# Optimization experiments

Hardware: AMD Instinct MI355X
Metric: run time of the kernel (lower is better)

The kernel has to match this reference:

```python
import jax, jax.numpy as jnp
import numpy as np

B, K, H = 512, 160, 256
ALPHA = 0.5          # fgw_alpha
TEMP = 2.0           # consistency temperature
MAX_SPAN = 30        # max_span_len
L_FGW, L_SPAN, L_CONS = 0.1, 0.5, 0.3


def setup_inputs() -> dict:
    key = jax.random.key(0)
    ks = jax.random.split(key, 12)
    gamma = jax.random.uniform(ks[0], (B, K, K), jnp.float32) / K  # transport-plan scale
    return {
        "en_node_emb": jax.random.normal(ks[1], (B, K, H), jnp.float32),
        "vi_node_emb": jax.random.normal(ks[2], (B, K, H), jnp.float32),
        "gamma": gamma,
        "D_en": jax.random.uniform(ks[3], (B, K, K), jnp.float32),
        "D_vi": jax.random.uniform(ks[4], (B, K, K), jnp.float32),
        "M": jax.random.uniform(ks[5], (B, K, K), jnp.float32),
        "en_start": jax.random.randint(ks[6], (B,), 0, K, jnp.int64 if jax.config.read('jax_enable_x64') else jnp.int32),
        "en_end": jax.random.randint(ks[7], (B,), 0, K, jnp.int64 if jax.config.read('jax_enable_x64') else jnp.int32),
        "w_start": jax.random.normal(ks[8], (H, 1), jnp.float32) * 0.02,
        "b_start": jnp.zeros((1,), jnp.float32),
        "w_end": jax.random.normal(ks[9], (H, 1), jnp.float32) * 0.02,
        "b_end": jnp.zeros((1,), jnp.float32),
    }


def _qa_head(emb, w_s, b_s, w_e, b_e):
    # emb: (B,K,H) -> logits (B,K)
    start = (emb @ w_s).squeeze(-1) + b_s
    end = (emb @ w_e).squeeze(-1) + b_e
    return start, end


def _ce(logits, labels):
    # mean cross-entropy, labels always valid after clamping
    logp = jax.nn.log_softmax(logits, axis=-1)
    return -jnp.take_along_axis(logp, labels[:, None], axis=-1).squeeze(-1)


def _fgw_loss(gamma, D_en, D_vi, M, alpha):
    w = jnp.sum(M * gamma, axis=(1, 2))
    p = gamma.sum(axis=2)  # (B,K)
    q = gamma.sum(axis=1)  # (B,K)
    gw1 = jnp.einsum('bij,bi,bj->b', D_en ** 2, p, p)
    gw2 = jnp.einsum('bij,bi,bj->b', D_vi ** 2, q, q)
    t = jnp.einsum('bik,bkl->bil', D_en, gamma)       # C1 @ g
    t = jnp.einsum('bil,bjl->bij', t, D_vi)           # (C1 @ g) @ C2^T
    gw3 = jnp.sum(t * gamma, axis=(1, 2))
    return jnp.mean(alpha * (gw1 + gw2 - 2.0 * gw3) + (1.0 - alpha) * w)


def _decode_span(gamma, en_start, en_end, k, max_span):
    # pseudo-label decode (no-grad in original) -> (B,) int start/end
    idx = jnp.arange(k)
    s = jnp.clip(en_start, 0, k - 1)
    e = jnp.maximum(s, jnp.clip(en_end, 0, k - 1))
    row_mask = (idx[None, :] >= s[:, None]) & (idx[None, :] <= e[:, None])  # (B,K)
    vi_score = jnp.einsum('bi,bij->bj', row_mask.astype(gamma.dtype), gamma)  # (B,K)
    pair = vi_score[:, :, None] + vi_score[:, None, :]  # (B, si, ei)
    span = idx[None, :] - idx[:, None]                  # ei - si
    valid = (span >= 0) & (span <= max_span)
    pair = jnp.where(valid[None], pair, -jnp.inf)
    flat = jnp.argmax(pair.reshape(pair.shape[0], -1), axis=-1)
    best_s, best_e = flat // k, flat % k
    unanswerable = (en_start == 0) & (en_end == 0)
    best_s = jnp.where(unanswerable, 0, best_s)
    best_e = jnp.where(unanswerable, 0, best_e)
    return best_s, best_e


def _kl_batchmean(vi_logp, en_logp):
    # KL(target=exp(en_logp) || vi) with torch kl_div(batchmean) semantics
    p = jnp.exp(en_logp)
    return jnp.sum(p * (en_logp - vi_logp)) / p.shape[0]


def reference(en_node_emb, vi_node_emb, gamma, D_en, D_vi, M, en_start, en_end,
              w_start, b_start, w_end, b_end):
    en_sl, en_el = _qa_head(en_node_emb, w_start, b_start, w_end, b_end)
    vi_sl, vi_el = _qa_head(vi_node_emb, w_start, b_start, w_end, b_end)

    # QA loss (EN supervised, positions clamped into [0, K-1])
    s_lab = jnp.clip(en_start, 0, K - 1)
    e_lab = jnp.clip(en_end, 0, K - 1)
    l_qa = (jnp.mean(_ce(en_sl, s_lab)) + jnp.mean(_ce(en_el, e_lab))) / 2.0

    # FGW alignment
    l_fgw = _fgw_loss(gamma, D_en, D_vi, M, ALPHA)

    # Span projection (pseudo labels via stop-gradient on gamma)
    ps, pe = _decode_span(jax.lax.stop_gradient(gamma), en_start, en_end, K, MAX_SPAN)
    answerable = ((en_start > 0) | (en_end > 0)).astype(jnp.float32)
    n_ans = jnp.sum(answerable)
    ce_span = (_ce(vi_sl, ps) + _ce(vi_el, pe)) / 2.0  # (B,)
    l_span = jnp.where(n_ans > 0, jnp.sum(ce_span * answerable) / jnp.maximum(n_ans, 1.0), 0.0)

    # Consistency (EN detached)
    en_s_log = jax.nn.log_softmax(jax.lax.stop_gradient(en_sl) / TEMP, axis=-1)
    en_e_log = jax.nn.log_softmax(jax.lax.stop_gradient(en_el) / TEMP, axis=-1)
    vi_s_log = jax.nn.log_softmax(vi_sl / TEMP, axis=-1)
    vi_e_log = jax.nn.log_softmax(vi_el / TEMP, axis=-1)
    l_cons = TEMP ** 2 * (_kl_batchmean(vi_s_log, en_s_log) + _kl_batchmean(vi_e_log, en_e_log)) / 2.0

    total = l_qa + L_FGW * l_fgw + L_SPAN * l_span + L_CONS * l_cons
    return total, l_qa, l_fgw, l_span, l_cons
```

## Files before the change

### kernel.cpp

```cpp
#include <hip/hip_runtime.h>

#define Bn 512
#define Kn 160
#define Hn 256
#define ALPHA 0.5f
#define MAX_SPAN 30
#define L_FGW 0.1f
#define L_SPAN 0.5f
#define L_CONS 0.3f
#define KP 16
#define NP 10

typedef __bf16 bf16x8 __attribute__((ext_vector_type(8)));
typedef float f32x16 __attribute__((ext_vector_type(16)));
typedef float f32x4v __attribute__((ext_vector_type(4)));

struct PhS {
  float prow[160][41];
  float qcol[16][160];
  float vcol[16][160];
  float psh[160], qsh[160], vscsh[160];
  float esh[160], eeh[160], vssh[160], veh[160];
  float wsh[16], g1sh[16], g2sh[16];
  float bv[256];
  int bidx[256];
  int pspe[2];
};
struct FgS {
  __bf16 sDen[2][2][Kn][8];
  __bf16 sG[2][2][Kn][8];
  __bf16 sGT[2][2][Kn][8];
  __bf16 sVT[2][2][Kn][8];
  float red[16];
};

__device__ __forceinline__ void wg_barrier() {
  asm volatile("s_waitcnt lgkmcnt(0)" ::: "memory");
  __builtin_amdgcn_s_barrier();
  __builtin_amdgcn_sched_barrier(0);
}

__global__ __launch_bounds__(1024, 4) void mega_k(
    const float* __restrict__ en, const float* __restrict__ vi,
    const float* __restrict__ w_s, const float* __restrict__ b_s,
    const float* __restrict__ w_e, const float* __restrict__ b_e,
    const float* __restrict__ gam, const float* __restrict__ M,
    const float* __restrict__ Den, const float* __restrict__ Dvi,
    const int* __restrict__ enst, const int* __restrict__ enen,
    float* __restrict__ sp1) {
  __shared__ __align__(16) char shraw[sizeof(PhS)];
  PhS& S = *(PhS*)shraw;
  FgS& F = *(FgS*)shraw;
  int b = blockIdx.x;
  int tid = threadIdx.x;
  int wv = tid >> 6, lane = tid & 63;
  const float* gam_b = gam + (size_t)b * 25600;
  const float* m_b   = M   + (size_t)b * 25600;
  const float* den_b = Den + (size_t)b * 25600;
  const float* dvi_b = Dvi + (size_t)b * 25600;
  int s0 = enst[b], e0 = enen[b];
  int s = min(max(s0, 0), Kn - 1);
  int e = max(s, min(max(e0, 0), Kn - 1));
  bool actA = tid < 640;
  int rm = tid / 40, c = tid - 40 * rm;

  float4 ws4 = *(const float4*)(w_s + lane * 4);
  float4 we4 = *(const float4*)(w_e + lane * 4);
  float bs0 = b_s[0], be0 = b_e[0];
  const float* en_b = en + (size_t)b * 40960;
  const float* vi_b = vi + (size_t)b * 40960;
  float q4[4] = {0.f,0.f,0.f,0.f}, v4[4] = {0.f,0.f,0.f,0.f};
  float wloc = 0.f;
  #pragma unroll
  for (int it = 0; it < 10; ++it) {
    int crow = wv * 10 + it;
    f32x4v ev = __builtin_nontemporal_load((const f32x4v*)(en_b + (size_t)crow * 256 + lane * 4));
    f32x4v vv = __builtin_nontemporal_load((const f32x4v*)(vi_b + (size_t)crow * 256 + lane * 4));
    if (actA) {
      int r = 16 * it + rm;
      float4 g = *(const float4*)(gam_b + (size_t)r * 160 + 4 * c);
      f32x4v m = __builtin_nontemporal_load((const f32x4v*)(m_b + (size_t)r * 160 + 4 * c));
      wloc += m[0]*g.x + m[1]*g.y + m[2]*g.z + m[3]*g.w;
      S.prow[r][c] = g.x + g.y + g.z + g.w;
      q4[0]+=g.x; q4[1]+=g.y; q4[2]+=g.z; q4[3]+=g.w;
      float f = (r >= s && r <= e) ? 1.f : 0.f;
      v4[0]+=f*g.x; v4[1]+=f*g.y; v4[2]+=f*g.z; v4[3]+=f*g.w;
    }
    float a0 = ev[0]*ws4.x + ev[1]*ws4.y + ev[2]*ws4.z + ev[3]*ws4.w;
    float a1 = ev[0]*we4.x + ev[1]*we4.y + ev[2]*we4.z + ev[3]*we4.w;
    float a2 = vv[0]*ws4.x + vv[1]*ws4.y + vv[2]*ws4.z + vv[3]*ws4.w;
    float a3 = vv[0]*we4.x + vv[1]*we4.y + vv[2]*we4.z + vv[3]*we4.w;
    #pragma unroll
    for (int o = 32; o; o >>= 1) {
      a0 += __shfl_xor(a0, o); a1 += __shfl_xor(a1, o);
      a2 += __shfl_xor(a2, o); a3 += __shfl_xor(a3, o);
    }
    if (lane == 0) {
      S.esh[crow] = a0 + bs0;  S.eeh[crow] = a1 + be0;
      S.vssh[crow] = a2 + bs0; S.veh[crow] = a3 + be0;
    }
  }
  if (actA) {
    #pragma unroll
    for (int j = 0; j < 4; ++j) { S.qcol[rm][4*c+j] = q4[j]; S.vcol[rm][4*c+j] = v4[j]; }
  }
  #pragma unroll
  for (int o = 32; o; o >>= 1) wloc += __shfl_xor(wloc, o);
  if (lane == 0) S.wsh[wv] = wloc;
  __syncthreads();
  if (tid < 160) {
    float sp = 0.f;
    #pragma unroll 8
    for (int c2 = 0; c2 < 40; ++c2) sp += S.prow[tid][c2];
    S.psh[tid] = sp;
    float sq = 0.f, sv = 0.f;
    #pragma unroll 4
    for (int k = 0; k < 16; ++k) { sq += S.qcol[k][tid]; sv += S.vcol[k][tid]; }
    S.qsh[tid] = sq;
    S.vscsh[tid] = sv;
  }
  __syncthreads();

  float g1loc = 0.f, g2loc = 0.f;
  if (actA) {
    float pc0=S.psh[4*c], pc1=S.psh[4*c+1], pc2=S.psh[4*c+2], pc3=S.psh[4*c+3];
    float qc0=S.qsh[4*c], qc1=S.qsh[4*c+1], qc2=S.qsh[4*c+2], qc3=S.qsh[4*c+3];
    #pragma unroll
    for (int k = 0; k < 10; ++k) {
      int r = 16 * k + rm;
      float4 d = *(const float4*)(den_b + (size_t)r * 160 + 4 * c);
      g1loc += S.psh[r] * (d.x*d.x*pc0 + d.y*d.y*pc1 + d.z*d.z*pc2 + d.w*d.w*pc3);
      float4 v = *(const float4*)(dvi_b + (size_t)r * 160 + 4 * c);
      g2loc += S.qsh[r] * (v.x*v.x*qc0 + v.y*v.y*qc1 + v.z*v.z*qc2 + v.w*v.w*qc3);
    }
  }
  #pragma unroll
  for (int o = 32; o; o >>= 1) { g1loc += __shfl_xor(g1loc, o); g2loc += __shfl_xor(g2loc, o); }
  if (lane == 0) { S.g1sh[wv] = g1loc; S.g2sh[wv] = g2loc; }
  __syncthreads();

  float best = -1e30f;
  int bfl = 0x7fffffff;
  if (tid < 160) {
    float vsi = S.vscsh[tid];
    int hi = min(tid + MAX_SPAN, Kn - 1);
    for (int ei = tid; ei <= hi; ++ei) {
      float v = vsi + S.vscsh[ei];
      if (v > best) { best = v; bfl = tid * Kn + ei; }
    }
  }
  if (tid < 256) { S.bv[tid] = best; S.bidx[tid] = bfl; }
  for (int st = 128; st > 0; st >>= 1) {
    __syncthreads();
    if (tid < st) {
      float v2 = S.bv[tid + st]; int i2 = S.bidx[tid + st];
      if (v2 > S.bv[tid] || (v2 == S.bv[tid] && i2 < S.bidx[tid])) { S.bv[tid] = v2; S.bidx[tid] = i2; }
    }
  }
  if (tid == 0) {
    int fl = S.bidx[0];
    int ps = fl / Kn, pe = fl - (fl / Kn) * Kn;
    if (s0 == 0 && e0 == 0) { ps = 0; pe = 0; }
    S.pspe[0] = ps; S.pspe[1] = pe;
    float sw = 0.f, s1 = 0.f, s2 = 0.f;
    #pragma unroll
    for (int i = 0; i < 16; ++i) { sw += S.wsh[i]; s1 += S.g1sh[i]; s2 += S.g2sh[i]; }
    float* o = sp1 + (size_t)b * 12;
    o[4] = sw; o[7] = s1; o[8] = s2;
  }
  __syncthreads();
  if (wv == 0) {
    float xes[3], xee[3], xvs[3], xve[3];
    #pragma unroll
    for (int j = 0; j < 3; ++j) {
      int idx = lane + 64 * j;
      bool val = idx < Kn;
      xes[j] = val ? S.esh[idx] : -1e30f;
      xee[j] = val ? S.eeh[idx] : -1e30f;
      xvs[j] = val ? S.vssh[idx] : -1e30f;
      xve[j] = val ? S.veh[idx] : -1e30f;
    }
    auto wlse = [&](float x0, float x1, float x2) -> float {
      float m = fmaxf(fmaxf(x0, x1), x2);
      #pragma unroll
      for (int o = 32; o; o >>= 1) m = fmaxf(m, __shfl_xor(m, o));
      float su = expf(x0 - m) + expf(x1 - m) + expf(x2 - m);
      #pragma unroll
      for (int o = 32; o; o >>= 1) su += __shfl_xor(su, o);
      return m + logf(su);
    };
    float l_es = wlse(xes[0], xes[1], xes[2]);
    float l_ee = wlse(xee[0], xee[1], xee[2]);
    float l_vs = wlse(xvs[0], xvs[1], xvs[2]);
    float l_ve = wlse(xve[0], xve[1], xve[2]);
    float lT_es = wlse(xes[0]*0.5f, xes[1]*0.5f, xes[2]*0.5f);
    float lT_ee = wlse(xee[0]*0.5f, xee[1]*0.5f, xee[2]*0.5f);
    float lT_vs = wlse(xvs[0]*0.5f, xvs[1]*0.5f, xvs[2]*0.5f);
    float lT_ve = wlse(xve[0]*0.5f, xve[1]*0.5f, xve[2]*0.5f);
    float kls = 0.f, kle = 0.f;
    #pragma unroll
    for (int j = 0; j < 3; ++j) {
      int idx = lane + 64 * j;
      if (idx < Kn) {
        float aa = xes[j]*0.5f - lT_es;
        float bb = xvs[j]*0.5f - lT_vs;
        kls += expf(aa) * (aa - bb);
        float cc = xee[j]*0.5f - lT_ee;
        float dd = xve[j]*0.5f - lT_ve;
        kle += expf(cc) * (cc - dd);
      }
    }
    #pragma unroll
    for (int o = 32; o; o >>= 1) { kls += __shfl_xor(kls, o); kle += __shfl_xor(kle, o); }
    if (lane == 0) {
      int sl = min(max(s0, 0), Kn - 1);
      int el = min(max(e0, 0), Kn - 1);
      float* o = sp1 + (size_t)b * 12;
      o[0] = l_es - S.esh[sl];
      o[1] = l_ee - S.eeh[el];
      o[2] = kls;
      o[3] = kle;
      bool answerable = (s0 > 0) || (e0 > 0);
      float ce = 0.5f * ((l_vs - S.vssh[S.pspe[0]]) + (l_ve - S.veh[S.pspe[1]]));
      o[5] = answerable ? ce : 0.f;
      o[6] = answerable ? 1.f : 0.f;
    }
  }
  __syncthreads();

  bool rm0 = tid < 640;
  const float* s0p;
  __bf16 *d00, *d01;
  if (rm0) {
    int op = tid >= 320 ? 1 : 0;
    int fr = tid - 320 * op;
    int cc = fr >= 160 ? 1 : 0;
    int r = fr - 160 * cc;
    s0p = (op ? gam_b : den_b) + (size_t)r * 160 + 8 * cc;
    d00 = op ? &F.sG[0][cc][r][0] : &F.sDen[0][cc][r][0];
    d01 = op ? &F.sG[1][cc][r][0] : &F.sDen[1][cc][r][0];
  } else {
    int f3 = tid - 640;
    int op = f3 >= 320 ? 1 : 0;
    int f4 = f3 - 320 * op;
    int cc = f4 >= 160 ? 1 : 0;
    int j = f4 - 160 * cc;
    s0p = (op ? dvi_b : gam_b) + (size_t)(8 * cc) * 160 + j;
    d00 = op ? &F.sVT[0][cc][j][0] : &F.sGT[0][cc][j][0];
    d01 = op ? &F.sVT[1][cc][j][0] : &F.sGT[1][cc][j][0];
  }
  bool act1 = tid < 256;
  int f5 = tid + 64;
  int cc1 = f5 >= 160 ? 1 : 0;
  int j1 = f5 - 160 * cc1;
  const float* s1p = dvi_b + (size_t)(8 * cc1) * 160 + j1;
  __bf16* d10 = &F.sVT[0][cc1][j1][0];
  __bf16* d11 = &F.sVT[1][cc1][j1][0];

  float vA0[8], vA1[8], vB0[8], vB1[8];
  auto load0 = [&](int p, float* v) {
    if (rm0) {
      const float* sp = s0p + p * KP;
      float4 x = *(const float4*)sp;
      float4 y = *(const float4*)(sp + 4);
      v[0]=x.x; v[1]=x.y; v[2]=x.z; v[3]=x.w;
      v[4]=y.x; v[5]=y.y; v[6]=y.z; v[7]=y.w;
    } else {
      const float* sp = s0p + (size_t)p * KP * 160;
      #pragma unroll
      for (int e2 = 0; e2 < 8; ++e2) v[e2] = sp[(size_t)e2 * 160];
    }
  };
  auto load1 = [&](int p, float* v) {
    if (!act1) return;
    const float* sp = s1p + (size_t)p * KP * 160;
    #pragma unroll
    for (int e2 = 0; e2 < 8; ++e2) v[e2] = sp[(size_t)e2 * 160];
  };
  auto wr = [&](const float* v0, const float* v1, __bf16* w0, __bf16* w1) {
    bf16x8 wv2;
    #pragma unroll
    for (int e2 = 0; e2 < 8; ++e2) wv2[e2] = (__bf16)v0[e2];
    *(bf16x8*)w0 = wv2;
    if (act1) {
      bf16x8 wv3;
      #pragma unroll
      for (int e2 = 0; e2 < 8; ++e2) wv3[e2] = (__bf16)v1[e2];
      *(bf16x8*)w1 = wv3;
    }
  };

  int ra = lane & 31, cc2 = lane >> 5;
  int t0 = wv;
  int ti0 = t0 / 5, tj0 = t0 - 5 * (t0 / 5);
  int rowa0 = ti0 * 32 + ra, rowb0 = tj0 * 32 + ra;
  int t1 = wv + 16;
  bool val1t = t1 < 25;
  int ti1 = t1 / 5, tj1 = t1 - 5 * (t1 / 5);
  int rowa1 = ti1 * 32 + ra, rowb1 = tj1 * 32 + ra;
  f32x16 acc10 = {}, acc20 = {}, acc11 = {}, acc21 = {};
  auto mf = [&](int BUF) {
    {
      bf16x8 a1 = *(const bf16x8*)&F.sDen[BUF][cc2][rowa0][0];
      bf16x8 b1 = *(const bf16x8*)&F.sGT[BUF][cc2][rowb0][0];
      bf16x8 a2 = *(const bf16x8*)&F.sG[BUF][cc2][rowa0][0];
      bf16x8 b2 = *(const bf16x8*)&F.sVT[BUF][cc2][rowb0][0];
      acc10 = __builtin_amdgcn_mfma_f32_32x32x16_bf16(a1, b1, acc10, 0, 0, 0);
      acc20 = __builtin_amdgcn_mfma_f32_32x32x16_bf16(a2, b2, acc20, 0, 0, 0);
    }
    if (val1t) {
      bf16x8 a1 = *(const bf16x8*)&F.sDen[BUF][cc2][rowa1][0];
      bf16x8 b1 = *(const bf16x8*)&F.sGT[BUF][cc2][rowb1][0];
      bf16x8 a2 = *(const bf16x8*)&F.sG[BUF][cc2][rowa1][0];
      bf16x8 b2 = *(const bf16x8*)&F.sVT[BUF][cc2][rowb1][0];
      acc11 = __builtin_amdgcn_mfma_f32_32x32x16_bf16(a1, b1, acc11, 0, 0, 0);
      acc21 = __builtin_amdgcn_mfma_f32_32x32x16_bf16(a2, b2, acc21, 0, 0, 0);
    }
  };

  load0(0, vA0); load1(0, vA1);
  load0(1, vB0); load1(1, vB1);
  wr(vA0, vA1, d00, d10);
  __syncthreads();
  for (int p = 0; p < NP; p += 2) {
    if (p + 2 < NP) { load0(p + 2, vA0); load1(p + 2, vA1); }
    mf(0);
    wr(vB0, vB1, d01, d11);
    wg_barrier();
    if (p + 3 < NP) { load0(p + 3, vB0); load1(p + 3, vB1); }
    mf(1);
    if (p + 2 < NP) wr(vA0, vA1, d00, d10);
    wg_barrier();
  }
  float g3 = 0.f;
  #pragma unroll
  for (int r2 = 0; r2 < 16; ++r2) g3 += acc10[r2] * acc20[r2];
  if (val1t) {
    #pragma unroll
    for (int r2 = 0; r2 < 16; ++r2) g3 += acc11[r2] * acc21[r2];
  }
  #pragma unroll
  for (int o = 32; o; o >>= 1) g3 += __shfl_xor(g3, o);
  if (lane == 0) F.red[wv] = g3;
  __syncthreads();
  if (tid == 0) {
    float s3 = 0.f;
    #pragma unroll
    for (int i = 0; i < 16; ++i) s3 += F.red[i];
    sp1[(size_t)b * 12 + 9] = s3;
  }
}

__global__ __launch_bounds__(512) void finalize_k(
    const float* __restrict__ sp1, float* __restrict__ out) {
  __shared__ float red[8][10];
  int tid = threadIdx.x;
  int wid = tid >> 6, lane = tid & 63;
  float v[10];
  const float* a = sp1 + (size_t)tid * 12;
  #pragma unroll
  for (int i = 0; i < 10; ++i) v[i] = a[i];
  #pragma unroll
  for (int i = 0; i < 10; ++i) {
    float s = v[i];
    #pragma unroll
    for (int o = 32; o; o >>= 1) s += __shfl_xor(s, o);
    v[i] = s;
  }
  if (lane == 0) {
    #pragma unroll
    for (int i = 0; i < 10; ++i) red[wid][i] = v[i];
  }
  __syncthreads();
  if (tid == 0) {
    float t[10];
    #pragma unroll
    for (int i = 0; i < 10; ++i) {
      float s = 0.f;
      #pragma unroll
      for (int w2 = 0; w2 < 8; ++w2) s += red[w2][i];
      t[i] = s;
    }
    float ce_s = t[0], ce_e = t[1], kls = t[2], kle = t[3];
    float w = t[4], spn = t[5], nans = t[6];
    float gw1 = t[7], gw2 = t[8], gw3 = t[9];
    float l_qa = (ce_s + ce_e) / (2.f * Bn);
    float l_fgw = (ALPHA * (gw1 + gw2 - 2.f * gw3) + (1.f - ALPHA) * w) / Bn;
    float l_span = (nans > 0.f) ? spn / fmaxf(nans, 1.f) : 0.f;
    float l_cons = 2.f * (kls + kle) / Bn;
    float total = l_qa + L_FGW * l_fgw + L_SPAN * l_span + L_CONS * l_cons;
    out[0] = total; out[1] = l_qa; out[2] = l_fgw; out[3] = l_span; out[4] = l_cons;
  }
}

extern "C" void kernel_launch(void* const* d_in, const int* in_sizes, int n_in,
                              void* d_out, int out_size, void* d_ws, size_t ws_size,
                              hipStream_t stream) {
  const float* en  = (const float*)d_in[0];
  const float* vi  = (const float*)d_in[1];
  const float* gam = (const float*)d_in[2];
  const float* Den = (const float*)d_in[3];
  const float* Dvi = (const float*)d_in[4];
  const float* M   = (const float*)d_in[5];
  const int* enst  = (const int*)d_in[6];
  const int* enen  = (const int*)d_in[7];
  const float* w_s = (const float*)d_in[8];
  const float* b_s = (const float*)d_in[9];
  const float* w_e = (const float*)d_in[10];
  const float* b_e = (const float*)d_in[11];
  float* sp1 = (float*)d_ws;
  float* out = (float*)d_out;

  mega_k<<<Bn, 1024, 0, stream>>>(en, vi, w_s, b_s, w_e, b_e, gam, M, Den, Dvi,
                                  enst, enen, sp1);
  finalize_k<<<1, 512, 0, stream>>>(sp1, out);
}
```

Measured before the change: 109.8 us.

## Fuse gw1/gw2 quadratic terms into the bf16 staging loads of D_en/D_vi

The separate pass that re-read D_en and D_vi from global memory to compute the p^T D^2 p and q^T D^2 q terms is removed. These terms are now accumulated inside the loaders that already stream D_en rows and D_vi columns into shared memory for the MFMA gw3 product. p and q are kept in dedicated shared arrays so they survive the shared-memory union reuse. This removes one full global read of two K×K matrices per batch, plus a barrier, at the cost of extra FMAs and shared reads inside the pipelined load phase.

```diff
diff --git a/kernel.cpp b/kernel.cpp
--- a/kernel.cpp
+++ b/kernel.cpp
@@ -19,9 +19,9 @@
   float prow[160][41];
   float qcol[16][160];
   float vcol[16][160];
-  float psh[160], qsh[160], vscsh[160];
+  float vscsh[160];
   float esh[160], eeh[160], vssh[160], veh[160];
-  float wsh[16], g1sh[16], g2sh[16];
+  float wsh[16];
   float bv[256];
   int bidx[256];
   int pspe[2];
@@ -31,7 +31,7 @@
   __bf16 sG[2][2][Kn][8];
   __bf16 sGT[2][2][Kn][8];
   __bf16 sVT[2][2][Kn][8];
-  float red[16];
+  float red[48];
 };
 
 __device__ __forceinline__ void wg_barrier() {
@@ -49,6 +49,8 @@
     const int* __restrict__ enst, const int* __restrict__ enen,
     float* __restrict__ sp1) {
   __shared__ __align__(16) char shraw[sizeof(PhS)];
+  __shared__ float psh_s[160];
+  __shared__ float qsh_s[160];
   PhS& S = *(PhS*)shraw;
   FgS& F = *(FgS*)shraw;
   int b = blockIdx.x;
@@ -112,31 +114,13 @@
     float sp = 0.f;
     #pragma unroll 8
     for (int c2 = 0; c2 < 40; ++c2) sp += S.prow[tid][c2];
-    S.psh[tid] = sp;
+    psh_s[tid] = sp;
     float sq = 0.f, sv = 0.f;
     #pragma unroll 4
     for (int k = 0; k < 16; ++k) { sq += S.qcol[k][tid]; sv += S.vcol[k][tid]; }
-    S.qsh[tid] = sq;
+    qsh_s[tid] = sq;
     S.vscsh[tid] = sv;
   }
-  __syncthreads();
-
-  float g1loc = 0.f, g2loc = 0.f;
-  if (actA) {
-    float pc0=S.psh[4*c], pc1=S.psh[4*c+1], pc2=S.psh[4*c+2], pc3=S.psh[4*c+3];
-    float qc0=S.qsh[4*c], qc1=S.qsh[4*c+1], qc2=S.qsh[4*c+2], qc3=S.qsh[4*c+3];
-    #pragma unroll
-    for (int k = 0; k < 10; ++k) {
-      int r = 16 * k + rm;
-      float4 d = *(const float4*)(den_b + (size_t)r * 160 + 4 * c);
-      g1loc += S.psh[r] * (d.x*d.x*pc0 + d.y*d.y*pc1 + d.z*d.z*pc2 + d.w*d.w*pc3);
-      float4 v = *(const float4*)(dvi_b + (size_t)r * 160 + 4 * c);
-      g2loc += S.qsh[r] * (v.x*v.x*qc0 + v.y*v.y*qc1 + v.z*v.z*qc2 + v.w*v.w*qc3);
-    }
-  }
-  #pragma unroll
-  for (int o = 32; o; o >>= 1) { g1loc += __shfl_xor(g1loc, o); g2loc += __shfl_xor(g2loc, o); }
-  if (lane == 0) { S.g1sh[wv] = g1loc; S.g2sh[wv] = g2loc; }
   __syncthreads();
 
   float best = -1e30f;
@@ -162,11 +146,10 @@
     int ps = fl / Kn, pe = fl - (fl / Kn) * Kn;
     if (s0 == 0 && e0 == 0) { ps = 0; pe = 0; }
     S.pspe[0] = ps; S.pspe[1] = pe;
-    float sw = 0.f, s1 = 0.f, s2 = 0.f;
-    #pragma unroll
-    for (int i = 0; i < 16; ++i) { sw += S.wsh[i]; s1 += S.g1sh[i]; s2 += S.g2sh[i]; }
-    float* o = sp1 + (size_t)b * 12;
-    o[4] = sw; o[7] = s1; o[8] = s2;
+    float sw = 0.f;
+    #pragma unroll
+    for (int i = 0; i < 16; ++i) sw += S.wsh[i];
+    sp1[(size_t)b * 12 + 4] = sw;
   }
   __syncthreads();
   if (wv == 0) {
@@ -231,6 +214,9 @@
   bool rm0 = tid < 640;
   const float* s0p;
   __bf16 *d00, *d01;
+  bool isDen0 = false, isVT0 = false;
+  float w0r = 0.f;
+  int cb0 = 0;
   if (rm0) {
     int op = tid >= 320 ? 1 : 0;
     int fr = tid - 320 * op;
@@ -239,6 +225,7 @@
     s0p = (op ? gam_b : den_b) + (size_t)r * 160 + 8 * cc;
     d00 = op ? &F.sG[0][cc][r][0] : &F.sDen[0][cc][r][0];
     d01 = op ? &F.sG[1][cc][r][0] : &F.sDen[1][cc][r][0];
+    if (!op) { isDen0 = true; w0r = psh_s[r]; cb0 = 8 * cc; }
   } else {
     int f3 = tid - 640;
     int op = f3 >= 320 ? 1 : 0;
@@ -248,6 +235,7 @@
     s0p = (op ? dvi_b : gam_b) + (size_t)(8 * cc) * 160 + j;
     d00 = op ? &F.sVT[0][cc][j][0] : &F.sGT[0][cc][j][0];
     d01 = op ? &F.sVT[1][cc][j][0] : &F.sGT[1][cc][j][0];
+    if (op) { isVT0 = true; w0r = qsh_s[j]; cb0 = 8 * cc; }
   }
   bool act1 = tid < 256;
   int f5 = tid + 64;
@@ -256,6 +244,9 @@
   const float* s1p = dvi_b + (size_t)(8 * cc1) * 160 + j1;
   __bf16* d10 = &F.sVT[0][cc1][j1][0];
   __bf16* d11 = &F.sVT[1][cc1][j1][0];
+  float w1r = act1 ? qsh_s[j1] : 0.f;
+  int cb1 = 8 * cc1;
+  float gw1a = 0.f, gw2a = 0.f;
 
   float vA0[8], vA1[8], vB0[8], vB1[8];
   auto load0 = [&](int p, float* v) {
@@ -265,10 +256,24 @@
       float4 y = *(const float4*)(sp + 4);
       v[0]=x.x; v[1]=x.y; v[2]=x.z; v[3]=x.w;
       v[4]=y.x; v[5]=y.y; v[6]=y.z; v[7]=y.w;
+      if (isDen0) {
+        const float* pw = psh_s + cb0 + 16 * p;
+        float t = 0.f;
+        #pragma unroll
+        for (int e2 = 0; e2 < 8; ++e2) t += v[e2] * v[e2] * pw[e2];
+        gw1a += w0r * t;
+      }
     } else {
       const float* sp = s0p + (size_t)p * KP * 160;
       #pragma unroll
       for (int e2 = 0; e2 < 8; ++e2) v[e2] = sp[(size_t)e2 * 160];
+      if (isVT0) {
+        const float* qw = qsh_s + cb0 + 16 * p;
+        float t = 0.f;
+        #pragma unroll
+        for (int e2 = 0; e2 < 8; ++e2) t += v[e2] * v[e2] * qw[e2];
+        gw2a += w0r * t;
+      }
     }
   };
   auto load1 = [&](int p, float* v) {
@@ -276,6 +281,11 @@
     const float* sp = s1p + (size_t)p * KP * 160;
     #pragma unroll
     for (int e2 = 0; e2 < 8; ++e2) v[e2] = sp[(size_t)e2 * 160];
+    const float* qw = qsh_s + cb1 + 16 * p;
+    float t = 0.f;
+    #pragma unroll
+    for (int e2 = 0; e2 < 8; ++e2) t += v[e2] * v[e2] * qw[e2];
+    gw2a += w1r * t;
   };
   auto wr = [&](const float* v0, const float* v1, __bf16* w0, __bf16* w1) {
     bf16x8 wv2;
@@ -340,14 +350,19 @@
     for (int r2 = 0; r2 < 16; ++r2) g3 += acc11[r2] * acc21[r2];
   }
   #pragma unroll
-  for (int o = 32; o; o >>= 1) g3 += __shfl_xor(g3, o);
-  if (lane == 0) F.red[wv] = g3;
+  for (int o = 32; o; o >>= 1) {
+    g3 += __shfl_xor(g3, o);
+    gw1a += __shfl_xor(gw1a, o);
+    gw2a += __shfl_xor(gw2a, o);
+  }
+  if (lane == 0) { F.red[wv] = g3; F.red[16 + wv] = gw1a; F.red[32 + wv] = gw2a; }
   __syncthreads();
   if (tid == 0) {
-    float s3 = 0.f;
-    #pragma unroll
-    for (int i = 0; i < 16; ++i) s3 += F.red[i];
-    sp1[(size_t)b * 12 + 9] = s3;
+    float s3 = 0.f, s1 = 0.f, s2 = 0.f;
+    #pragma unroll
+    for (int i = 0; i < 16; ++i) { s3 += F.red[i]; s1 += F.red[16 + i]; s2 += F.red[32 + i]; }
+    float* o = sp1 + (size_t)b * 12;
+    o[7] = s1; o[8] = s2; o[9] = s3;
   }
 }
 
```

Result: no change. 109.0 us (median of 2 runs) (-0.7%).
